# Kernel tuning notes

Measured on AMD Instinct MI355X. Metric: run time of the kernel, lower is better.

## Reference

```python
import jax, jax.numpy as jnp
import numpy as np

L, H, C, HS, V, BS = 4, 4, 1024, 256, 32000, 1024  # layers, heads, n_embd, head_size, vocab, block_size
B, T = 4, 1024
EPS = 1e-5

def _ln(x, g, b):
    mu = jnp.mean(x, axis=-1, keepdims=True)
    var = jnp.mean((x - mu) ** 2, axis=-1, keepdims=True)
    return (x - mu) / jnp.sqrt(var + EPS) * g + b

def setup_inputs() -> dict:
    key = jax.random.key(0)
    ks = iter(jax.random.split(key, 32))
    s = 0.02
    inp = {
        'idx': jax.random.randint(next(ks), (B, T), 0, V),
        'tok_emb': jax.random.normal(next(ks), (V, C), jnp.float32) * s,
        'pos_emb': jax.random.normal(next(ks), (BS, C), jnp.float32) * s,
        'wq': jax.random.normal(next(ks), (L, H, C, HS), jnp.float32) * s,
        'wk': jax.random.normal(next(ks), (L, H, C, HS), jnp.float32) * s,
        'wv': jax.random.normal(next(ks), (L, H, C, HS), jnp.float32) * s,
        'proj_w': jax.random.normal(next(ks), (L, C, C), jnp.float32) * s,
        'proj_b': jnp.zeros((L, C), jnp.float32),
        'ln1_g': jnp.ones((L, C), jnp.float32),
        'ln1_b': jnp.zeros((L, C), jnp.float32),
        'ln2_g': jnp.ones((L, C), jnp.float32),
        'ln2_b': jnp.zeros((L, C), jnp.float32),
        'ff_w1': jax.random.normal(next(ks), (L, C, 4 * C), jnp.float32) * s,
        'ff_b1': jnp.zeros((L, 4 * C), jnp.float32),
        'ff_w2': jax.random.normal(next(ks), (L, 4 * C, C), jnp.float32) * s,
        'ff_b2': jnp.zeros((L, C), jnp.float32),
        'lnf_g': jnp.ones((C,), jnp.float32),
        'lnf_b': jnp.zeros((C,), jnp.float32),
        'head_w': jax.random.normal(next(ks), (C, V), jnp.float32) * s,
        'head_b': jnp.zeros((V,), jnp.float32),
    }
    return inp

def reference(idx, tok_emb, pos_emb, wq, wk, wv, proj_w, proj_b, ln1_g, ln1_b,
              ln2_g, ln2_b, ff_w1, ff_b1, ff_w2, ff_b2, lnf_g, lnf_b, head_w, head_b):
    b, t = idx.shape
    x = tok_emb[idx] + pos_emb[:t]  # (B,T,C)
    causal = jnp.tril(jnp.ones((t, t), bool))
    inv_sqrt_c = np.float32(1.0 / np.sqrt(C))  # NOTE: original scales by sqrt(n_embd), not head_size
    for l in range(L):
        xn = _ln(x, ln1_g[l], ln1_b[l])
        q = jnp.einsum('btc,hcd->bhtd', xn, wq[l])
        k = jnp.einsum('bsc,hcd->bhsd', xn, wk[l])
        v = jnp.einsum('bsc,hcd->bhsd', xn, wv[l])
        scores = jnp.einsum('bhtd,bhsd->bhts', q, k)
        scores = jnp.where(causal, scores, -jnp.inf) * inv_sqrt_c
        # original: F.softmax(xdot, dim=1) on (B,T,T) -> normalize over the QUERY axis
        alpha = jax.nn.softmax(scores, axis=2)
        y = jnp.einsum('bhts,bhsd->bhtd', alpha, v)
        y = y.transpose(0, 2, 1, 3).reshape(b, t, C)  # concat heads
        x = x + y @ proj_w[l] + proj_b[l]
        xn2 = _ln(x, ln2_g[l], ln2_b[l])
        h = jax.nn.relu(xn2 @ ff_w1[l] + ff_b1[l])
        x = x + h @ ff_w2[l] + ff_b2[l]
    x = _ln(x, lnf_g, lnf_b)
    logits = x @ head_w + head_b  # (B,T,V)
    return logits
```

## Files before the change

### kernel.cpp

```cpp
#include <hip/hip_runtime.h>


#define C_  1024
#define T_  1024
#define HS_ 256
#define H_  4
#define L_  4
#define V_  32000
#define B_  4
#define M_  4096

typedef __attribute__((ext_vector_type(8))) short  bfx8;
typedef __attribute__((ext_vector_type(4))) float  fx4;
typedef __attribute__((ext_vector_type(4))) unsigned short usx4;

__device__ __forceinline__ unsigned short f2bf(float f) {
  unsigned int u = __builtin_bit_cast(unsigned int, f);
  u += 0x7fffu + ((u >> 16) & 1u);
  return (unsigned short)(u >> 16);
}
__device__ __forceinline__ float bf2f(unsigned short u) {
  return __builtin_bit_cast(float, ((unsigned int)u) << 16);
}

__device__ __forceinline__ void gload16(const unsigned short* g, unsigned short* l) {
  __builtin_amdgcn_global_load_lds(
      (const __attribute__((address_space(1))) unsigned int*)g,
      (__attribute__((address_space(3))) unsigned int*)l, 16, 0, 0);
}

template<int BIAS, int RES, int RELU, int OUTBF>
__global__ __launch_bounds__(256, 2) void gemm_bf16(
    const unsigned short* __restrict__ A, const unsigned short* __restrict__ Bm,
    const float* __restrict__ bias, const float* __restrict__ res,
    void* __restrict__ out,
    int M, int N, int K, int lda, int ldb, int ldc,
    long sA, long sB, long sC1, long sC2, int zShift, long rowOuter)
{
  __shared__ unsigned short As[128 * 32];
  __shared__ unsigned short Bs[128 * 32];
  const int z = blockIdx.z;
  A  += (long)z * sA;
  Bm += (long)z * sB;
  const long outOff = ((long)(z >> zShift)) * sC1 + (long)(z & ((1 << zShift) - 1)) * sC2;
  const int m0 = blockIdx.x * 128, n0 = blockIdx.y * 128;
  const int tid = threadIdx.x;
  const int lane = tid & 63, wave = tid >> 6;
  const int wm = (wave >> 1) * 64, wn = (wave & 1) * 64;
  const int fr = lane & 15, kb = lane >> 4;
  const int sr = lane >> 2;
  const int csw = (((lane & 3) ^ ((lane >> 3) & 3)) << 3);
  const int aco = ((kb ^ ((lane >> 1) & 3)) << 3);

  fx4 acc[4][4] = {};

  for (int k0 = 0; k0 < K; k0 += 32) {
    #pragma unroll
    for (int i = 0; i < 2; ++i) {
      const int c = wave * 2 + i;
      gload16(A  + (long)(m0 + c * 16 + sr) * lda + k0 + csw, &As[c * 512]);
      gload16(Bm + (long)(n0 + c * 16 + sr) * ldb + k0 + csw, &Bs[c * 512]);
    }
    __syncthreads();
    bfx8 af[4], bf[4];
    #pragma unroll
    for (int i = 0; i < 4; ++i)
      af[i] = *reinterpret_cast<const bfx8*>(&As[(wm + i * 16 + fr) * 32 + aco]);
    #pragma unroll
    for (int j = 0; j < 4; ++j)
      bf[j] = *reinterpret_cast<const bfx8*>(&Bs[(wn + j * 16 + fr) * 32 + aco]);
    #pragma unroll
    for (int i = 0; i < 4; ++i)
      #pragma unroll
      for (int j = 0; j < 4; ++j)
        acc[i][j] = __builtin_amdgcn_mfma_f32_16x16x32_bf16(af[i], bf[j], acc[i][j], 0, 0, 0);
    __syncthreads();
  }

  const float* resp = res;
  if (RES) resp += outOff;
  const int rbase = (lane >> 4) * 4;
  #pragma unroll
  for (int j = 0; j < 4; ++j) {
    const int n = n0 + wn + j * 16 + fr;
    float bv = 0.f;
    if (BIAS) bv = bias[n];
    #pragma unroll
    for (int i = 0; i < 4; ++i) {
      #pragma unroll
      for (int r = 0; r < 4; ++r) {
        const int m = m0 + wm + i * 16 + rbase + r;
        const long off = outOff + ((long)(m >> 10)) * rowOuter + (long)(m & 1023) * ldc + n;
        float val = acc[i][j][r] + bv;
        if (RELU) val = fmaxf(val, 0.f);
        if (RES) val += resp[((long)(m >> 10)) * rowOuter + (long)(m & 1023) * ldc + n];
        if (OUTBF) ((unsigned short*)out)[off] = f2bf(val);
        else       ((float*)out)[off] = val;
      }
    }
  }
}

#define BAR() __builtin_amdgcn_s_barrier()
#define LGKM() { asm volatile("s_waitcnt lgkmcnt(0)" ::: "memory"); \
                 __builtin_amdgcn_sched_barrier(0); }
#define VM6()  asm volatile("s_waitcnt vmcnt(6)" ::: "memory")
#define RD_A(p, kh, rh) { _Pragma("unroll") for (int i = 0; i < 4; ++i) \
  af[i] = *reinterpret_cast<const bfx8*>(&S[((p)*2+(kh))*8192 + (wr*128 + (rh)*64 + i*16 + fr)*32 + aco]); }
#define RD_B(p, kh) { _Pragma("unroll") for (int j = 0; j < 4; ++j) \
  bf[j] = *reinterpret_cast<const bfx8*>(&S[32768 + ((p)*2+(kh))*8192 + (wc*64 + j*16 + fr)*32 + aco]); }
#define MM16(rh) { __builtin_amdgcn_s_setprio(1); \
  _Pragma("unroll") for (int i = 0; i < 4; ++i) { _Pragma("unroll") for (int j = 0; j < 4; ++j) \
    acc[(rh)*4+i][j] = __builtin_amdgcn_mfma_f32_16x16x32_bf16(af[i], bf[j], acc[(rh)*4+i][j], 0, 0, 0); } \
  __builtin_amdgcn_s_setprio(0); }

template<int BIAS, int RELU, int OUTBF, int EPI>
__global__ __launch_bounds__(512, 2) void gemm256(
    const unsigned short* __restrict__ A, const unsigned short* __restrict__ Bm,
    const float* __restrict__ bias, void* __restrict__ out,
    int K, int lda, int ldb, int ldc,
    long sA, long sB, long sC1, long rowOuter)
{
  __shared__ unsigned short S[65536];
  const int z = blockIdx.z;
  A  += (long)z * sA;
  Bm += (long)z * sB;
  const long outOff = (long)z * sC1;
  const int m0 = blockIdx.x * 256, n0 = blockIdx.y * 256;
  const int tid = threadIdx.x;
  const int lane = tid & 63, wave = tid >> 6;
  const int wr = wave >> 2, wc = wave & 3;
  const int fr = lane & 15, kb = lane >> 4;
  const int srow = lane >> 2;
  const int csw = (((lane & 3) ^ (((lane >> 5) & 1) << 1)) << 3);
  const int aco = ((kb ^ (((fr >> 3) & 1) << 1)) << 3);
  const int NT = K >> 6;
  const int NI = NT >> 1;

  fx4 acc[8][4] = {};
  bfx8 af[4], bf[4];

  auto stA = [&](int tau, int kh) {
    const int tc = tau < NT ? tau : NT - 1;
    const unsigned short* src = A + (long)(m0 + wave * 16 + srow) * lda + tc * 64 + kh * 32 + csw;
    unsigned short* d = &S[((tau & 1) * 2 + kh) * 8192 + wave * 512];
    gload16(src, d);
    gload16(src + (long)128 * lda, d + 4096);
  };
  auto stB = [&](int tau, int kh) {
    const int tc = tau < NT ? tau : NT - 1;
    const unsigned short* src = Bm + (long)(n0 + wave * 16 + srow) * ldb + tc * 64 + kh * 32 + csw;
    unsigned short* d = &S[32768 + ((tau & 1) * 2 + kh) * 8192 + wave * 512];
    gload16(src, d);
    gload16(src + (long)128 * ldb, d + 4096);
  };

  stA(0, 0); stB(0, 0); stA(0, 1); stB(0, 1); stA(1, 0); stB(1, 0);
  asm volatile("s_waitcnt vmcnt(8)" ::: "memory");
  BAR();

  for (int t = 0; t < NI; ++t) {
    const int u = 2 * t;
    RD_A(0, 0, 0); RD_B(0, 0); stA(u + 1, 1);
    BAR(); LGKM(); MM16(0); BAR();
    RD_A(0, 0, 1); stB(u + 1, 1);
    BAR(); LGKM(); MM16(1); VM6(); BAR();
    RD_A(0, 1, 0); RD_B(0, 1); stA(u + 2, 0);
    BAR(); LGKM(); MM16(0); BAR();
    RD_A(0, 1, 1); stB(u + 2, 0);
    BAR(); LGKM(); MM16(1); VM6(); BAR();
    RD_A(1, 0, 0); RD_B(1, 0); stA(u + 2, 1);
    BAR(); LGKM(); MM16(0); BAR();
    RD_A(1, 0, 1); stB(u + 2, 1);
    BAR(); LGKM(); MM16(1); VM6(); BAR();
    RD_A(1, 1, 0); RD_B(1, 1); stA(u + 3, 0);
    BAR(); LGKM(); MM16(0); BAR();
    RD_A(1, 1, 1); stB(u + 3, 0);
    BAR(); LGKM(); MM16(1); VM6(); BAR();
  }
  asm volatile("s_waitcnt vmcnt(0)" ::: "memory");
  BAR();

  const int rbase = (lane >> 4) * 4;
  if (EPI == 1) {
    const int sel = n0 >> 10, h = (n0 >> 8) & 3;
    unsigned short* dst = (unsigned short*)out
        + (long)sel * ((long)B_ * H_ * T_ * HS_) + (long)h * T_ * HS_;
    #pragma unroll
    for (int j = 0; j < 4; ++j) {
      const int d = wc * 64 + j * 16 + fr;
      #pragma unroll
      for (int i = 0; i < 8; ++i) {
        #pragma unroll
        for (int r = 0; r < 4; ++r) {
          const int m = m0 + wr * 128 + i * 16 + rbase + r;
          const int bq = m >> 10, tq = m & 1023;
          dst[(long)bq * H_ * T_ * HS_ + (long)tq * HS_ + d] = f2bf(acc[i][j][r]);
        }
      }
    }
  } else {
    float* lf = (float*)S;
    #pragma unroll
    for (int jh = 0; jh < 2; ++jh) {
      #pragma unroll
      for (int jj = 0; jj < 2; ++jj)
        #pragma unroll
        for (int i = 0; i < 8; ++i)
          #pragma unroll
          for (int r = 0; r < 4; ++r) {
            const int row = i * 16 + rbase + r;
            const int cw = (jj * 16 + fr) ^ ((row & 7) << 2);
            lf[wave * 4096 + row * 32 + cw] = acc[i][jh * 2 + jj][r];
          }
      #pragma unroll
      for (int rs = 0; rs < 16; ++rs) {
        const int row = rs * 8 + (lane >> 3);
        const int c0 = (lane & 7) * 4;
        const int cw = c0 ^ ((row & 7) << 2);
        fx4 val = *reinterpret_cast<const fx4*>(&lf[wave * 4096 + row * 32 + cw]);
        const int n = n0 + wc * 64 + jh * 32 + c0;
        const int m = m0 + wr * 128 + row;
        const long off = outOff + ((long)(m >> 10)) * rowOuter + (long)(m & 1023) * ldc + n;
        if (BIAS) {
          const float4 bb = *reinterpret_cast<const float4*>(bias + n);
          val[0] += bb.x; val[1] += bb.y; val[2] += bb.z; val[3] += bb.w;
        }
        if (RELU) {
          val[0] = fmaxf(val[0], 0.f); val[1] = fmaxf(val[1], 0.f);
          val[2] = fmaxf(val[2], 0.f); val[3] = fmaxf(val[3], 0.f);
        }
        if (OUTBF) {
          usx4 o = { f2bf(val[0]), f2bf(val[1]), f2bf(val[2]), f2bf(val[3]) };
          *reinterpret_cast<usx4*>((unsigned short*)out + off) = o;
        } else {
          *reinterpret_cast<float4*>((float*)out + off) = *(const float4*)&val;
        }
      }
      __builtin_amdgcn_sched_barrier(0);
    }
  }
}

template<typename TIN>
__global__ __launch_bounds__(256) void transpose_k(const TIN* __restrict__ src,
    unsigned short* __restrict__ dst, int R, int Cc, int zShiftT, long sOuter) {
  __shared__ float ts[64][65];
  const long zb = blockIdx.z;
  src += zb * (long)R * Cc;
  dst += (zb >> zShiftT) * sOuter + (zb & ((1 << zShiftT) - 1)) * ((long)R * Cc);
  const int r0 = blockIdx.y * 64, c0 = blockIdx.x * 64;
  const int tr = threadIdx.x >> 4;
  const int tc = (threadIdx.x & 15) * 4;
  #pragma unroll
  for (int it = 0; it < 4; ++it) {
    const int r = tr + it * 16;
    float4 v;
    if constexpr (sizeof(TIN) == 4) {
      v = *reinterpret_cast<const float4*>(src + (long)(r0 + r) * Cc + c0 + tc);
    } else {
      usx4 u = *reinterpret_cast<const usx4*>(src + (long)(r0 + r) * Cc + c0 + tc);
      v.x = bf2f(u[0]); v.y = bf2f(u[1]); v.z = bf2f(u[2]); v.w = bf2f(u[3]);
    }
    ts[r][tc + 0] = v.x; ts[r][tc + 1] = v.y; ts[r][tc + 2] = v.z; ts[r][tc + 3] = v.w;
  }
  __syncthreads();
  #pragma unroll
  for (int it = 0; it < 4; ++it) {
    const int cj = tr + it * 16;
    usx4 o = { f2bf(ts[tc + 0][cj]), f2bf(ts[tc + 1][cj]),
               f2bf(ts[tc + 2][cj]), f2bf(ts[tc + 3][cj]) };
    *reinterpret_cast<usx4*>(dst + (long)(c0 + cj) * R + r0 + tc) = o;
  }
}

__global__ __launch_bounds__(256) void embed_k(const int* __restrict__ idx,
                                               const float* __restrict__ tok,
                                               const float* __restrict__ pos,
                                               float* __restrict__ x) {
  const int row = blockIdx.x;
  const int t = row & (T_ - 1);
  const int id = idx[row];
  const int c = threadIdx.x * 4;
  const float4 a = *reinterpret_cast<const float4*>(tok + (long)id * C_ + c);
  const float4 p = *reinterpret_cast<const float4*>(pos + (long)t * C_ + c);
  float4 ov = { a.x + p.x, a.y + p.y, a.z + p.z, a.w + p.w };
  *reinterpret_cast<float4*>(x + (long)row * C_ + c) = ov;
}

__global__ __launch_bounds__(256) void ln_k(const float* __restrict__ x,
                                            const float* __restrict__ g,
                                            const float* __restrict__ b,
                                            unsigned short* __restrict__ o) {
  __shared__ float red[8];
  const int row = blockIdx.x;
  const int c = threadIdx.x * 4;
  const float4 v = *reinterpret_cast<const float4*>(x + (long)row * C_ + c);
  float s1 = v.x + v.y + v.z + v.w;
  float s2 = v.x * v.x + v.y * v.y + v.z * v.z + v.w * v.w;
  #pragma unroll
  for (int off = 32; off; off >>= 1) {
    s1 += __shfl_xor(s1, off, 64);
    s2 += __shfl_xor(s2, off, 64);
  }
  const int lane = threadIdx.x & 63, w = threadIdx.x >> 6;
  if (lane == 0) { red[w] = s1; red[4 + w] = s2; }
  __syncthreads();
  s1 = red[0] + red[1] + red[2] + red[3];
  s2 = red[4] + red[5] + red[6] + red[7];
  const float mu = s1 * (1.f / C_);
  float var = s2 * (1.f / C_) - mu * mu;
  var = fmaxf(var, 0.f);
  const float inv = rsqrtf(var + 1e-5f);
  const float4 gg = *reinterpret_cast<const float4*>(g + c);
  const float4 bb = *reinterpret_cast<const float4*>(b + c);
  usx4 ov;
  ov[0] = f2bf((v.x - mu) * inv * gg.x + bb.x);
  ov[1] = f2bf((v.y - mu) * inv * gg.y + bb.y);
  ov[2] = f2bf((v.z - mu) * inv * gg.z + bb.z);
  ov[3] = f2bf((v.w - mu) * inv * gg.w + bb.w);
  *reinterpret_cast<usx4*>(o + (long)row * C_ + c) = ov;
}

__global__ __launch_bounds__(256) void colsm_k(const unsigned short* __restrict__ a,
                                               unsigned short* __restrict__ aT) {
  __shared__ float red[8];
  const int row = blockIdx.x;
  const int s = row & (T_ - 1);
  const unsigned short* p = a + (long)row * T_;
  const int t0 = threadIdx.x * 4;
  const usx4 u = *reinterpret_cast<const usx4*>(p + t0);
  const float scale = 0.03125f;
  float vals[4];
  float m = -1e30f;
  #pragma unroll
  for (int j = 0; j < 4; ++j) {
    vals[j] = (t0 + j >= s) ? bf2f(u[j]) * scale : -1e30f;
    m = fmaxf(m, vals[j]);
  }
  #pragma unroll
  for (int off = 32; off; off >>= 1) m = fmaxf(m, __shfl_xor(m, off, 64));
  const int lane = threadIdx.x & 63, w = threadIdx.x >> 6;
  if (lane == 0) red[w] = m;
  __syncthreads();
  m = fmaxf(fmaxf(red[0], red[1]), fmaxf(red[2], red[3]));
  __syncthreads();
  float e[4], sum = 0.f;
  #pragma unroll
  for (int j = 0; j < 4; ++j) {
    e[j] = (t0 + j >= s) ? __expf(vals[j] - m) : 0.f;
    sum += e[j];
  }
  #pragma unroll
  for (int off = 32; off; off >>= 1) sum += __shfl_xor(sum, off, 64);
  if (lane == 0) red[w] = sum;
  __syncthreads();
  sum = red[0] + red[1] + red[2] + red[3];
  const float inv = 1.f / sum;
  usx4 ov = { f2bf(e[0] * inv), f2bf(e[1] * inv), f2bf(e[2] * inv), f2bf(e[3] * inv) };
  *reinterpret_cast<usx4*>(aT + (long)row * T_ + t0) = ov;
}

extern "C" void kernel_launch(void* const* d_in, const int* in_sizes, int n_in,
                              void* d_out, int out_size, void* d_ws, size_t ws_size,
                              hipStream_t stream) {
  const int*   idx    = (const int*)d_in[0];
  const float* tok    = (const float*)d_in[1];
  const float* pos    = (const float*)d_in[2];
  const float* wq     = (const float*)d_in[3];
  const float* wk     = (const float*)d_in[4];
  const float* wv     = (const float*)d_in[5];
  const float* proj_w = (const float*)d_in[6];
  const float* proj_b = (const float*)d_in[7];
  const float* ln1_g  = (const float*)d_in[8];
  const float* ln1_b  = (const float*)d_in[9];
  const float* ln2_g  = (const float*)d_in[10];
  const float* ln2_b  = (const float*)d_in[11];
  const float* ff_w1  = (const float*)d_in[12];
  const float* ff_b1  = (const float*)d_in[13];
  const float* ff_w2  = (const float*)d_in[14];
  const float* ff_b2  = (const float*)d_in[15];
  const float* lnf_g  = (const float*)d_in[16];
  const float* lnf_b  = (const float*)d_in[17];
  const float* head_w = (const float*)d_in[18];
  const float* head_b = (const float*)d_in[19];
  float* outp = (float*)d_out;

  typedef unsigned short us;
  char* w = (char*)d_ws;
  float* x    = (float*)(w + 0);
  us* xn      = (us*)(w + 16777216);
  us* qkv     = (us*)(w + 25165824);
  us* kptr    = qkv + 4194304;
  us* vptr    = qkv + 8388608;
  us* vT      = (us*)(w + 50331648);
  us* yc      = (us*)(w + 58720256);
  us* sc      = (us*)(w + 67108864);
  us* headT   = (us*)(w + 67108864);
  us* alpha   = (us*)(w + 100663296);
  us* aT      = (us*)(w + 134217728);
  us* hidden  = aT;
  us* wqkvT   = (us*)(w + 167772160);
  us* projT   = (us*)(w + 192937984);
  us* ff1T    = (us*)(w + 201326592);
  us* ff2T    = (us*)(w + 234881024);
  if (ws_size < (size_t)268435456) return;

  const long HHC = (long)H_ * HS_ * C_;
  transpose_k<float><<<dim3(HS_/64, C_/64, L_*H_), 256, 0, stream>>>(wq, wqkvT,           C_, HS_, 2, 3*HHC);
  transpose_k<float><<<dim3(HS_/64, C_/64, L_*H_), 256, 0, stream>>>(wk, wqkvT + HHC,     C_, HS_, 2, 3*HHC);
  transpose_k<float><<<dim3(HS_/64, C_/64, L_*H_), 256, 0, stream>>>(wv, wqkvT + 2*HHC,   C_, HS_, 2, 3*HHC);
  transpose_k<float><<<dim3(C_/64, C_/64, L_), 256, 0, stream>>>(proj_w, projT, C_, C_, 0, (long)C_*C_);
  transpose_k<float><<<dim3(4*C_/64, C_/64, L_), 256, 0, stream>>>(ff_w1, ff1T, C_, 4*C_, 0, (long)C_*4*C_);
  transpose_k<float><<<dim3(C_/64, 4*C_/64, L_), 256, 0, stream>>>(ff_w2, ff2T, 4*C_, C_, 0, (long)4*C_*C_);

  embed_k<<<M_, 256, 0, stream>>>(idx, tok, pos, x);

  for (int l = 0; l < L_; ++l) {
    ln_k<<<M_, 256, 0, stream>>>(x, ln1_g + l * C_, ln1_b + l * C_, xn);

    dim3 gqkv(M_/256, 3*C_/256, 1);
    gemm256<0,0,1,1><<<gqkv, 512, 0, stream>>>(xn, wqkvT + l * 3 * HHC, nullptr, qkv,
        C_, C_, C_, 0, 0, 0, 0, 0);

    dim3 gs(T_/256, T_/256, B_*H_);
    gemm256<0,0,1,0><<<gs, 512, 0, stream>>>(kptr, qkv, nullptr, sc,
        HS_, HS_, HS_, T_, (long)T_*HS_, (long)T_*HS_, (long)T_*T_, 0);

    colsm_k<<<B_*H_*T_, 256, 0, stream>>>(sc, aT);

    transpose_k<us><<<dim3(T_/64, T_/64, B_*H_), 256, 0, stream>>>(aT, alpha, T_, T_, 0, (long)T_*T_);
    transpose_k<us><<<dim3(HS_/64, T_/64, B_*H_), 256, 0, stream>>>(vptr, vT, T_, HS_, 0, (long)T_*HS_);

    dim3 gp(T_/128, HS_/128, B_*H_);
    gemm_bf16<0,0,0,1><<<gp, 256, 0, stream>>>(alpha, vT, nullptr, nullptr, yc,
        T_, HS_, T_, T_, T_, C_, (long)T_*T_, (long)HS_*T_, (long)T_*C_, HS_, 2, (long)T_*C_);

    dim3 gj(M_/128, C_/128, 1);
    gemm_bf16<1,1,0,0><<<gj, 256, 0, stream>>>(yc, projT + (long)l*C_*C_, proj_b + l*C_, x, x,
        M_, C_, C_, C_, C_, C_, 0, 0, 0, 0, 0, (long)T_*C_);

    ln_k<<<M_, 256, 0, stream>>>(x, ln2_g + l * C_, ln2_b + l * C_, xn);

    dim3 g1(M_/256, 4*C_/256, 1);
    gemm256<1,1,1,0><<<g1, 512, 0, stream>>>(xn, ff1T + (long)l*4*C_*C_, ff_b1 + (long)l*4*C_,
        hidden, C_, C_, C_, 4*C_, 0, 0, 0, (long)1024*4*C_);

    dim3 g2(M_/128, C_/128, 1);
    gemm_bf16<1,1,0,0><<<g2, 256, 0, stream>>>(hidden, ff2T + (long)l*C_*4*C_, ff_b2 + l*C_, x, x,
        M_, C_, 4*C_, 4*C_, 4*C_, C_, 0, 0, 0, 0, 0, (long)T_*C_);
  }

  ln_k<<<M_, 256, 0, stream>>>(x, lnf_g, lnf_b, xn);

  transpose_k<float><<<dim3(V_/64, C_/64, 1), 256, 0, stream>>>(head_w, headT, C_, V_, 0, (long)C_*V_);

  dim3 gh(M_/256, V_/256, 1);
  gemm256<1,0,0,0><<<gh, 512, 0, stream>>>(xn, headT, head_b, outp,
      C_, C_, C_, V_, 0, 0, 0, (long)1024*V_);
}
```

Baseline: 1.610 ms.

## Double-buffer LDS fragment registers to overlap reads with MFMA in GEMM loop

Restructures the 256x256 GEMM main loop so LDS-to-register fragment reads for the next sub-step are issued while MFMAs run on the current fragments, using ping-pong register sets (afa/afb, bf0/bf1). Global prefetch depth grows to two full k-tiles, and the per-step barrier count drops from two to one. The intent is to hide LDS latency and cut synchronisation stalls. The cost is higher register pressure at 2 blocks per CU, plus a risk of LDS reuse hazards if the new stage ordering is wrong.

```diff
diff --git a/kernel.cpp b/kernel.cpp
--- a/kernel.cpp
+++ b/kernel.cpp
@@ -104,14 +104,22 @@
 #define BAR() __builtin_amdgcn_s_barrier()
 #define LGKM() { asm volatile("s_waitcnt lgkmcnt(0)" ::: "memory"); \
                  __builtin_amdgcn_sched_barrier(0); }
-#define VM6()  asm volatile("s_waitcnt vmcnt(6)" ::: "memory")
-#define RD_A(p, kh, rh) { _Pragma("unroll") for (int i = 0; i < 4; ++i) \
-  af[i] = *reinterpret_cast<const bfx8*>(&S[((p)*2+(kh))*8192 + (wr*128 + (rh)*64 + i*16 + fr)*32 + aco]); }
-#define RD_B(p, kh) { _Pragma("unroll") for (int j = 0; j < 4; ++j) \
-  bf[j] = *reinterpret_cast<const bfx8*>(&S[32768 + ((p)*2+(kh))*8192 + (wc*64 + j*16 + fr)*32 + aco]); }
-#define MM16(rh) { __builtin_amdgcn_s_setprio(1); \
+#define VM8()  asm volatile("s_waitcnt vmcnt(8)" ::: "memory")
+#define STA(tau, kh) { const int tc = (tau) < NT ? (tau) : NT - 1; \
+  const unsigned short* src = A + (long)(m0 + wave * 16 + srow) * lda + tc * 64 + (kh) * 32 + csw; \
+  unsigned short* d = &S[(((tau) & 1) * 2 + (kh)) * 8192 + wave * 512]; \
+  gload16(src, d); gload16(src + (long)128 * lda, d + 4096); }
+#define STB(tau, kh) { const int tc = (tau) < NT ? (tau) : NT - 1; \
+  const unsigned short* src = Bm + (long)(n0 + wave * 16 + srow) * ldb + tc * 64 + (kh) * 32 + csw; \
+  unsigned short* d = &S[32768 + (((tau) & 1) * 2 + (kh)) * 8192 + wave * 512]; \
+  gload16(src, d); gload16(src + (long)128 * ldb, d + 4096); }
+#define RDA(dst, par, kh, rh) { _Pragma("unroll") for (int i = 0; i < 4; ++i) \
+  dst[i] = *reinterpret_cast<const bfx8*>(&S[((par)*2+(kh))*8192 + (wr*128 + (rh)*64 + i*16 + fr)*32 + aco]); }
+#define RDB(dst, par, kh) { _Pragma("unroll") for (int j = 0; j < 4; ++j) \
+  dst[j] = *reinterpret_cast<const bfx8*>(&S[32768 + ((par)*2+(kh))*8192 + (wc*64 + j*16 + fr)*32 + aco]); }
+#define MM(rh, afx, bfx) { __builtin_amdgcn_s_setprio(1); \
   _Pragma("unroll") for (int i = 0; i < 4; ++i) { _Pragma("unroll") for (int j = 0; j < 4; ++j) \
-    acc[(rh)*4+i][j] = __builtin_amdgcn_mfma_f32_16x16x32_bf16(af[i], bf[j], acc[(rh)*4+i][j], 0, 0, 0); } \
+    acc[(rh)*4+i][j] = __builtin_amdgcn_mfma_f32_16x16x32_bf16(afx[i], bfx[j], acc[(rh)*4+i][j], 0, 0, 0); } \
   __builtin_amdgcn_s_setprio(0); }
 
 template<int BIAS, int RELU, int OUTBF, int EPI>
@@ -138,45 +146,26 @@
   const int NI = NT >> 1;
 
   fx4 acc[8][4] = {};
-  bfx8 af[4], bf[4];
-
-  auto stA = [&](int tau, int kh) {
-    const int tc = tau < NT ? tau : NT - 1;
-    const unsigned short* src = A + (long)(m0 + wave * 16 + srow) * lda + tc * 64 + kh * 32 + csw;
-    unsigned short* d = &S[((tau & 1) * 2 + kh) * 8192 + wave * 512];
-    gload16(src, d);
-    gload16(src + (long)128 * lda, d + 4096);
-  };
-  auto stB = [&](int tau, int kh) {
-    const int tc = tau < NT ? tau : NT - 1;
-    const unsigned short* src = Bm + (long)(n0 + wave * 16 + srow) * ldb + tc * 64 + kh * 32 + csw;
-    unsigned short* d = &S[32768 + ((tau & 1) * 2 + kh) * 8192 + wave * 512];
-    gload16(src, d);
-    gload16(src + (long)128 * ldb, d + 4096);
-  };
-
-  stA(0, 0); stB(0, 0); stA(0, 1); stB(0, 1); stA(1, 0); stB(1, 0);
-  asm volatile("s_waitcnt vmcnt(8)" ::: "memory");
+  bfx8 afa[4], afb[4], bf0[4], bf1[4];
+
+  STB(0, 0); STA(0, 0); STB(0, 1); STA(0, 1);
+  STB(1, 0); STA(1, 0); STB(1, 1); STA(1, 1);
+  VM8();
+  BAR();
+  RDA(afa, 0, 0, 0); RDB(bf1, 0, 0);
+  LGKM();
   BAR();
 
   for (int t = 0; t < NI; ++t) {
     const int u = 2 * t;
-    RD_A(0, 0, 0); RD_B(0, 0); stA(u + 1, 1);
-    BAR(); LGKM(); MM16(0); BAR();
-    RD_A(0, 0, 1); stB(u + 1, 1);
-    BAR(); LGKM(); MM16(1); VM6(); BAR();
-    RD_A(0, 1, 0); RD_B(0, 1); stA(u + 2, 0);
-    BAR(); LGKM(); MM16(0); BAR();
-    RD_A(0, 1, 1); stB(u + 2, 0);
-    BAR(); LGKM(); MM16(1); VM6(); BAR();
-    RD_A(1, 0, 0); RD_B(1, 0); stA(u + 2, 1);
-    BAR(); LGKM(); MM16(0); BAR();
-    RD_A(1, 0, 1); stB(u + 2, 1);
-    BAR(); LGKM(); MM16(1); VM6(); BAR();
-    RD_A(1, 1, 0); RD_B(1, 1); stA(u + 3, 0);
-    BAR(); LGKM(); MM16(0); BAR();
-    RD_A(1, 1, 1); stB(u + 3, 0);
-    BAR(); LGKM(); MM16(1); VM6(); BAR();
+    STB(u + 2, 0); RDA(afb, 0, 0, 1);                 MM(0, afa, bf1); LGKM(); BAR();
+    STA(u + 2, 0); RDA(afa, 0, 1, 0); RDB(bf0, 0, 1); MM(1, afb, bf1); LGKM(); VM8(); BAR();
+    STB(u + 2, 1); RDA(afb, 0, 1, 1);                 MM(0, afa, bf0); LGKM(); BAR();
+    STA(u + 2, 1); RDA(afa, 1, 0, 0); RDB(bf1, 1, 0); MM(1, afb, bf0); LGKM(); VM8(); BAR();
+    STB(u + 3, 0); RDA(afb, 1, 0, 1);                 MM(0, afa, bf1); LGKM(); BAR();
+    STA(u + 3, 0); RDA(afa, 1, 1, 0); RDB(bf0, 1, 1); MM(1, afb, bf1); LGKM(); VM8(); BAR();
+    STB(u + 3, 1); RDA(afb, 1, 1, 1);                 MM(0, afa, bf0); LGKM(); BAR();
+    STA(u + 3, 1); RDA(afa, 0, 0, 0); RDB(bf1, 0, 0); MM(1, afb, bf0); LGKM(); VM8(); BAR();
   }
   asm volatile("s_waitcnt vmcnt(0)" ::: "memory");
   BAR();
```

After: 1.605 ms. About the same (-0.3%).
